# Kernel optimization log

Measured on AMD Instinct MI355X. Metric: run time of the kernel, lower is better.

## Reference

```python
import jax, jax.numpy as jnp
import numpy as np

PI = 3.141592653589793
WINDOW = 16


def multi_pose(y):
    """Intensity-moment pose extraction (MultiPoseExtraction).
    y: [..., h, w] nonnegative intensities.
    Returns mu [...,2,1] (x,y centroid in pixel coords), U [...,2,2] with
    row 0 = principal eigenvector, and eigenvalues (L1, L2), L1 >= L2,
    via the same closed-form 2x2 eigen solve used in congregate_pose."""
    h, w = y.shape[-2], y.shape[-1]
    X = jnp.arange(w, dtype=y.dtype)            # column (x) coordinate
    Y = jnp.arange(h, dtype=y.dtype)[:, None]   # row (y) coordinate
    tot = jnp.sum(y, axis=(-2, -1), keepdims=True)
    p = y / (tot + 1e-8)
    mu_x = jnp.sum(p * X, axis=(-2, -1))
    mu_y = jnp.sum(p * Y, axis=(-2, -1))
    dx = X - mu_x[..., None, None]
    dy = Y - mu_y[..., None, None]
    cxx = jnp.sum(p * dx * dx, axis=(-2, -1))
    cyy = jnp.sum(p * dy * dy, axis=(-2, -1))
    cxy = jnp.sum(p * dx * dy, axis=(-2, -1))
    tr = cxx + cyy
    det = cxx * cyy - cxy * cxy
    disc = jnp.sqrt(jax.nn.relu(tr * tr - 4.0 * det))
    L1 = (tr + disc) / 2.0
    L2 = (tr - disc) / 2.0
    v1 = jnp.stack([L1 - cyy, cxy], axis=-1)
    v1 = v1 / jnp.maximum(jnp.linalg.norm(v1, axis=-1, keepdims=True), 1e-12)
    v2 = jnp.stack([-v1[..., 1], v1[..., 0]], axis=-1)
    U = jnp.stack([v1, v2], axis=-2)            # [...,2,2], U[...,0,:] = v1
    mu = jnp.stack([mu_x, mu_y], axis=-1)[..., None]  # [...,2,1]
    return mu, U, (L1, L2)


def deep_hog_forward(x, window):
    B, C, H, W = x.shape  # C == 1
    w = window
    mean = jnp.mean(x)
    # nn.Unfold with kernel=stride=w -> non-overlapping windows, row-major order
    blocks = x.reshape(B, H // w, w, W // w, w)
    blocks = blocks.transpose(0, 1, 3, 2, 4).reshape(B, -1, w, w)  # [B, L, w, w]
    block_means = blocks.mean(axis=(-2, -1))                        # [B, L]

    mu_global, _, _ = multi_pose(x)             # [B, 1, 2, 1]
    mu_W, U, (L1, L2) = multi_pose(blocks)      # [B,L,2,1], [B,L,2,2], [B,L]

    conf = ((L1 / L2)[..., None] - 1.0) * (block_means[..., None] / mean)
    conf = 20.0 * (jax.nn.sigmoid(conf) - 0.5)  # [B, L, 1]
    orient = U[:, :, 0, :] * conf               # [B, L, 2]

    # congregate_pose: closed-form top eigenvector of sum of outer products
    M = jnp.einsum('bli,blj->bij', orient, orient)  # [B,2,2]
    T_ = M[:, 0, 0] + M[:, 1, 1]
    D = M[:, 0, 0] * M[:, 1, 1] - M[:, 0, 1] * M[:, 1, 0]
    L1g = (T_ + jnp.sqrt(jax.nn.relu(T_ * T_ - 4.0 * D))) / 2.0
    v1 = jnp.stack([L1g - M[:, 1, 1], M[:, 1, 0]], axis=1)
    V = v1 / jnp.maximum(jnp.linalg.norm(v1, axis=1, keepdims=True), 1e-12)  # [B,2]

    output = jnp.concatenate([mu_W[:, :, :, 0], orient], axis=2)  # [B, L, 4]
    U_global = V[:, None, :]                                      # [B, 1, 2]

    # anti_pose_transformation
    eps = 1e-4
    rot_lambda = jnp.fmod(
        jnp.arctan2(U_global[:, 0, 1], U_global[:, 0, 0] + eps) + 2.0 * PI, PI)
    diff = PI / 2.0 - rot_lambda                 # [B]
    c, s = jnp.cos(diff), jnp.sin(diff)
    R = jnp.stack([jnp.stack([c, -s], axis=-1),
                   jnp.stack([s, c], axis=-1)], axis=-2)  # [B,2,2]
    mu = mu_global[:, 0, :, 0]                            # [B,2]
    mu_T = mu * jnp.array([1.0 / W, 1.0 / H], x.dtype) - 0.5   # normalize, - mu_R
    mu_T = mu_T * jnp.array([2.0, -2.0], x.dtype)               # flip_y_loc
    theta = jnp.concatenate([R, mu_T[:, :, None]], axis=2)      # [B,2,3]

    return output, blocks, mu_global, U_global, theta


def setup_inputs() -> dict:
    key = jax.random.key(0)
    x = jax.random.uniform(key, (64, 1, 1024, 1024), dtype=jnp.float32)
    return {"x": x}


def reference(x):
    return deep_hog_forward(x, WINDOW)
```

## Files before the change

kernel.cpp:

```cpp
#include <hip/hip_runtime.h>
#include <math.h>

#define PI_F 3.14159265358979323846f

#define OUT_OUTPUT   0
#define OUT_BLOCKS   1048576
#define OUT_MU       68157440
#define OUT_UG       68157568
#define OUT_THETA    68157696

#define WS_A   0
#define WS_B   1048576
#define WS_IMG 2097152
#define WS_M   2097216

__global__ __launch_bounds__(256) void k1_blocks(const float* __restrict__ x,
                                                 float* __restrict__ out,
                                                 float* __restrict__ ws) {
    __shared__ float lds[16 * 264];
    const int t = threadIdx.x;
    const int colstrip = blockIdx.x;
    const int rowstrip = blockIdx.y;
    const int b = blockIdx.z;

    const float4* x4 = reinterpret_cast<const float4*>(x)
                     + (size_t)b * 262144 + (size_t)rowstrip * 4096 + colstrip * 64;
    #pragma unroll
    for (int i = 0; i < 4; ++i) {
        int pos4 = i * 256 + t;
        int row  = pos4 >> 6;
        int col4 = pos4 & 63;
        float4 v = x4[row * 256 + col4];
        int ib = col4 >> 2;
        int c4 = (col4 & 3) << 2;
        *reinterpret_cast<float4*>(&lds[ib * 264 + row * 16 + c4]) = v;
    }
    __syncthreads();

    float* outB = out + OUT_BLOCKS
                + ((size_t)b * 4096 + rowstrip * 64 + colstrip * 16) * 256;
    #pragma unroll
    for (int i = 0; i < 4; ++i) {
        int pos4 = i * 256 + t;
        int ib  = pos4 >> 6;
        int off = (pos4 & 63) << 2;
        float4 v = *reinterpret_cast<const float4*>(&lds[ib * 264 + off]);
        reinterpret_cast<float4*>(outB)[pos4] = v;
    }

    const int ib = t >> 4;
    const int c  = t & 15;
    float s0 = 0.f, s1y = 0.f, s2yy = 0.f;
    #pragma unroll
    for (int r = 0; r < 16; ++r) {
        float v  = lds[ib * 264 + r * 16 + c];
        float rf = (float)r;
        s0   += v;
        s1y  += rf * v;
        s2yy += rf * rf * v;
    }
    float cf   = (float)c;
    float s1x  = cf * s0;
    float s2xx = cf * cf * s0;
    float s2xy = cf * s1y;
    #pragma unroll
    for (int m = 1; m <= 8; m <<= 1) {
        s0   += __shfl_xor(s0,   m);
        s1x  += __shfl_xor(s1x,  m);
        s1y  += __shfl_xor(s1y,  m);
        s2xx += __shfl_xor(s2xx, m);
        s2yy += __shfl_xor(s2yy, m);
        s2xy += __shfl_xor(s2xy, m);
    }
    if (c == 0) {
        float denom = s0 + 1e-8f;
        float inv   = 1.0f / denom;
        float mu_x = s1x * inv, mu_y = s1y * inv;
        float cxx = (s2xx - 2.f * mu_x * s1x + mu_x * mu_x * s0) * inv;
        float cyy = (s2yy - 2.f * mu_y * s1y + mu_y * mu_y * s0) * inv;
        float cxy = (s2xy - mu_x * s1y - mu_y * s1x + mu_x * mu_y * s0) * inv;
        float tr  = cxx + cyy;
        float det = cxx * cyy - cxy * cxy;
        float disc = sqrtf(fmaxf(tr * tr - 4.f * det, 0.f));
        float L1 = 0.5f * (tr + disc), L2 = 0.5f * (tr - disc);
        float v1x = L1 - cyy, v1y = cxy;
        float n = fmaxf(sqrtf(v1x * v1x + v1y * v1y), 1e-12f);
        v1x /= n; v1y /= n;
        float rm1 = L1 / L2 - 1.0f;

        int l = rowstrip * 64 + colstrip * 16 + ib;
        size_t gbl = (size_t)b * 4096 + l;
        out[OUT_OUTPUT + gbl * 4 + 0] = mu_x;
        out[OUT_OUTPUT + gbl * 4 + 1] = mu_y;

        float X0 = (float)(colstrip * 256 + ib * 16);
        float Y0 = (float)(rowstrip * 16);
        float4 wa = make_float4(v1x, v1y, rm1, s0 * (1.f / 256.f));
        float4 wb = make_float4(s0, s1x + X0 * s0, s1y + Y0 * s0, 0.f);
        reinterpret_cast<float4*>(ws + WS_A)[gbl] = wa;
        reinterpret_cast<float4*>(ws + WS_B)[gbl] = wb;
    }
}

__global__ __launch_bounds__(256) void k2_global(float* __restrict__ out,
                                                 float* __restrict__ ws) {
    __shared__ float red[12];
    const int b = blockIdx.x;
    const int t = threadIdx.x;
    float s0 = 0.f, gx = 0.f, gy = 0.f;
    const float4* wb = reinterpret_cast<const float4*>(ws + WS_B) + (size_t)b * 4096;
    #pragma unroll
    for (int k = 0; k < 16; ++k) {
        float4 v = wb[t + k * 256];
        s0 += v.x; gx += v.y; gy += v.z;
    }
    #pragma unroll
    for (int m = 1; m <= 32; m <<= 1) {
        s0 += __shfl_xor(s0, m);
        gx += __shfl_xor(gx, m);
        gy += __shfl_xor(gy, m);
    }
    int w = t >> 6;
    if ((t & 63) == 0) { red[w] = s0; red[4 + w] = gx; red[8 + w] = gy; }
    __syncthreads();
    if (t == 0) {
        float S0 = red[0] + red[1] + red[2] + red[3];
        float GX = red[4] + red[5] + red[6] + red[7];
        float GY = red[8] + red[9] + red[10] + red[11];
        float inv = 1.0f / (S0 + 1e-8f);
        out[OUT_MU + b * 2 + 0] = GX * inv;
        out[OUT_MU + b * 2 + 1] = GY * inv;
        ws[WS_IMG + b] = S0;
    }
}

__global__ __launch_bounds__(256) void k3_orient(float* __restrict__ out,
                                                 float* __restrict__ ws) {
    __shared__ float red[12];
    const int b = blockIdx.x;
    const int t = threadIdx.x;
    float tot = 0.f;
    #pragma unroll
    for (int k = 0; k < 64; ++k) tot += ws[WS_IMG + k];
    float invmean = 67108864.0f / tot;
    float m00 = 0.f, m01 = 0.f, m11 = 0.f;
    const float4* wa = reinterpret_cast<const float4*>(ws + WS_A) + (size_t)b * 4096;
    #pragma unroll
    for (int k = 0; k < 16; ++k) {
        int l = t + k * 256;
        float4 v = wa[l];
        float z = v.z * (v.w * invmean);
        float conf = 20.f * (1.f / (1.f + expf(-z)) - 0.5f);
        float ox = v.x * conf, oy = v.y * conf;
        size_t gbl = (size_t)b * 4096 + l;
        *reinterpret_cast<float2*>(&out[OUT_OUTPUT + gbl * 4 + 2]) = make_float2(ox, oy);
        m00 += ox * ox; m01 += ox * oy; m11 += oy * oy;
    }
    #pragma unroll
    for (int m = 1; m <= 32; m <<= 1) {
        m00 += __shfl_xor(m00, m);
        m01 += __shfl_xor(m01, m);
        m11 += __shfl_xor(m11, m);
    }
    int w = t >> 6;
    if ((t & 63) == 0) { red[w] = m00; red[4 + w] = m01; red[8 + w] = m11; }
    __syncthreads();
    if (t == 0) {
        float M00 = red[0] + red[1] + red[2] + red[3];
        float M01 = red[4] + red[5] + red[6] + red[7];
        float M11 = red[8] + red[9] + red[10] + red[11];
        reinterpret_cast<float4*>(ws + WS_M)[b] = make_float4(M00, M01, M11, 0.f);
    }
}

__global__ void k4_theta(float* __restrict__ out, const float* __restrict__ ws) {
    int b = threadIdx.x;
    if (b >= 64) return;
    float4 M = reinterpret_cast<const float4*>(ws + WS_M)[b];
    float T = M.x + M.z;
    float D = M.x * M.z - M.y * M.y;
    float L1g = 0.5f * (T + sqrtf(fmaxf(T * T - 4.f * D, 0.f)));
    float vx = L1g - M.z, vy = M.y;
    float n = fmaxf(sqrtf(vx * vx + vy * vy), 1e-12f);
    float Vx = vx / n, Vy = vy / n;
    out[OUT_UG + b * 2 + 0] = Vx;
    out[OUT_UG + b * 2 + 1] = Vy;
    float rot = fmodf(atan2f(Vy, Vx + 1e-4f) + 2.f * PI_F, PI_F);
    float diff = 0.5f * PI_F - rot;
    float cc = cosf(diff), ssn = sinf(diff);
    float mu_x = out[OUT_MU + b * 2 + 0];
    float mu_y = out[OUT_MU + b * 2 + 1];
    float mtx = (mu_x * (1.f / 1024.f) - 0.5f) * 2.f;
    float mty = (mu_y * (1.f / 1024.f) - 0.5f) * (-2.f);
    out[OUT_THETA + b * 6 + 0] = cc;
    out[OUT_THETA + b * 6 + 1] = -ssn;
    out[OUT_THETA + b * 6 + 2] = mtx;
    out[OUT_THETA + b * 6 + 3] = ssn;
    out[OUT_THETA + b * 6 + 4] = cc;
    out[OUT_THETA + b * 6 + 5] = mty;
}

extern "C" void kernel_launch(void* const* d_in, const int* in_sizes, int n_in,
                              void* d_out, int out_size, void* d_ws, size_t ws_size,
                              hipStream_t stream) {
    const float* x = (const float*)d_in[0];
    float* out = (float*)d_out;
    float* ws  = (float*)d_ws;
    dim3 g1(4, 64, 64);
    k1_blocks<<<g1, 256, 0, stream>>>(x, out, ws);
    k2_global<<<64, 256, 0, stream>>>(out, ws);
    k3_orient<<<64, 256, 0, stream>>>(out, ws);
    k4_theta<<<1, 64, 0, stream>>>(out, ws);
}
```

Before: 447.1 us.

## Fuse global reduction, orientation and theta kernels; pre-reduce per-workgroup partials

Folds k2, k3 and k4 into a single kernel and has k1 reduce its 16 block partials in LDS into one per-workgroup entry, so the global stage reads 16K partials instead of 262K. The blocks copy now uses nontemporal stores, and output rows are written as full float4 rows rather than split writes. The aim is to remove two launches and cut workspace traffic. The cost is that every workgroup redundantly reads all partials to get the global total. The main k1 traffic, dominated by the 256 MB input read and 256 MB write, is unchanged.

```diff
diff --git a/kernel.cpp b/kernel.cpp
--- a/kernel.cpp
+++ b/kernel.cpp
@@ -2,6 +2,8 @@
 #include <math.h>
 
 #define PI_F 3.14159265358979323846f
+
+typedef float f4 __attribute__((ext_vector_type(4)));
 
 #define OUT_OUTPUT   0
 #define OUT_BLOCKS   1048576
@@ -10,30 +12,30 @@
 #define OUT_THETA    68157696
 
 #define WS_A   0
-#define WS_B   1048576
-#define WS_IMG 2097152
-#define WS_M   2097216
+#define WS_C   1048576
+#define WS_P   1310720
 
 __global__ __launch_bounds__(256) void k1_blocks(const float* __restrict__ x,
                                                  float* __restrict__ out,
                                                  float* __restrict__ ws) {
     __shared__ float lds[16 * 264];
+    __shared__ float redP[3][16];
     const int t = threadIdx.x;
     const int colstrip = blockIdx.x;
     const int rowstrip = blockIdx.y;
     const int b = blockIdx.z;
 
-    const float4* x4 = reinterpret_cast<const float4*>(x)
-                     + (size_t)b * 262144 + (size_t)rowstrip * 4096 + colstrip * 64;
+    const f4* x4 = reinterpret_cast<const f4*>(x)
+                 + (size_t)b * 262144 + (size_t)rowstrip * 4096 + colstrip * 64;
     #pragma unroll
     for (int i = 0; i < 4; ++i) {
         int pos4 = i * 256 + t;
         int row  = pos4 >> 6;
         int col4 = pos4 & 63;
-        float4 v = x4[row * 256 + col4];
+        f4 v = x4[row * 256 + col4];
         int ib = col4 >> 2;
         int c4 = (col4 & 3) << 2;
-        *reinterpret_cast<float4*>(&lds[ib * 264 + row * 16 + c4]) = v;
+        *reinterpret_cast<f4*>(&lds[ib * 264 + row * 16 + c4]) = v;
     }
     __syncthreads();
 
@@ -44,8 +46,8 @@
         int pos4 = i * 256 + t;
         int ib  = pos4 >> 6;
         int off = (pos4 & 63) << 2;
-        float4 v = *reinterpret_cast<const float4*>(&lds[ib * 264 + off]);
-        reinterpret_cast<float4*>(outB)[pos4] = v;
+        f4 v = *reinterpret_cast<const f4*>(&lds[ib * 264 + off]);
+        __builtin_nontemporal_store(v, reinterpret_cast<f4*>(outB) + pos4);
     }
 
     const int ib = t >> 4;
@@ -90,70 +92,78 @@
 
         int l = rowstrip * 64 + colstrip * 16 + ib;
         size_t gbl = (size_t)b * 4096 + l;
-        out[OUT_OUTPUT + gbl * 4 + 0] = mu_x;
-        out[OUT_OUTPUT + gbl * 4 + 1] = mu_y;
+        f4 wa = {v1x, v1y, mu_x, mu_y};
+        reinterpret_cast<f4*>(ws + WS_A)[gbl] = wa;
+        ws[WS_C + gbl] = rm1 * (s0 * (1.f / 256.f));
 
         float X0 = (float)(colstrip * 256 + ib * 16);
         float Y0 = (float)(rowstrip * 16);
-        float4 wa = make_float4(v1x, v1y, rm1, s0 * (1.f / 256.f));
-        float4 wb = make_float4(s0, s1x + X0 * s0, s1y + Y0 * s0, 0.f);
-        reinterpret_cast<float4*>(ws + WS_A)[gbl] = wa;
-        reinterpret_cast<float4*>(ws + WS_B)[gbl] = wb;
+        redP[0][ib] = s0;
+        redP[1][ib] = s1x + X0 * s0;
+        redP[2][ib] = s1y + Y0 * s0;
+    }
+    __syncthreads();
+    if (t == 0) {
+        float S0 = 0.f, GX = 0.f, GY = 0.f;
+        #pragma unroll
+        for (int i = 0; i < 16; ++i) { S0 += redP[0][i]; GX += redP[1][i]; GY += redP[2][i]; }
+        int wg = (b << 8) | (rowstrip << 2) | colstrip;
+        reinterpret_cast<f4*>(ws + WS_P)[wg] = (f4){S0, GX, GY, 0.f};
     }
 }
 
-__global__ __launch_bounds__(256) void k2_global(float* __restrict__ out,
-                                                 float* __restrict__ ws) {
-    __shared__ float red[12];
+__global__ __launch_bounds__(256) void k23_orient(float* __restrict__ out,
+                                                  const float* __restrict__ ws) {
+    __shared__ float red[16];
+    __shared__ float bc[1];
     const int b = blockIdx.x;
     const int t = threadIdx.x;
-    float s0 = 0.f, gx = 0.f, gy = 0.f;
-    const float4* wb = reinterpret_cast<const float4*>(ws + WS_B) + (size_t)b * 4096;
-    #pragma unroll
-    for (int k = 0; k < 16; ++k) {
-        float4 v = wb[t + k * 256];
-        s0 += v.x; gx += v.y; gy += v.z;
+
+    const f4* wp = reinterpret_cast<const f4*>(ws + WS_P);
+    float tS0 = 0.f, iS0 = 0.f, igx = 0.f, igy = 0.f;
+    #pragma unroll
+    for (int k = 0; k < 64; ++k) {
+        f4 v = wp[k * 256 + t];
+        tS0 += v.x;
+        if (k == b) { iS0 += v.x; igx += v.y; igy += v.z; }
     }
     #pragma unroll
     for (int m = 1; m <= 32; m <<= 1) {
-        s0 += __shfl_xor(s0, m);
-        gx += __shfl_xor(gx, m);
-        gy += __shfl_xor(gy, m);
-    }
-    int w = t >> 6;
-    if ((t & 63) == 0) { red[w] = s0; red[4 + w] = gx; red[8 + w] = gy; }
-    __syncthreads();
+        tS0 += __shfl_xor(tS0, m);
+        iS0 += __shfl_xor(iS0, m);
+        igx += __shfl_xor(igx, m);
+        igy += __shfl_xor(igy, m);
+    }
+    const int w = t >> 6;
+    if ((t & 63) == 0) { red[w] = tS0; red[4 + w] = iS0; red[8 + w] = igx; red[12 + w] = igy; }
+    __syncthreads();
+    float mu_x = 0.f, mu_y = 0.f;
     if (t == 0) {
-        float S0 = red[0] + red[1] + red[2] + red[3];
-        float GX = red[4] + red[5] + red[6] + red[7];
-        float GY = red[8] + red[9] + red[10] + red[11];
-        float inv = 1.0f / (S0 + 1e-8f);
-        out[OUT_MU + b * 2 + 0] = GX * inv;
-        out[OUT_MU + b * 2 + 1] = GY * inv;
-        ws[WS_IMG + b] = S0;
-    }
-}
-
-__global__ __launch_bounds__(256) void k3_orient(float* __restrict__ out,
-                                                 float* __restrict__ ws) {
-    __shared__ float red[12];
-    const int b = blockIdx.x;
-    const int t = threadIdx.x;
-    float tot = 0.f;
-    #pragma unroll
-    for (int k = 0; k < 64; ++k) tot += ws[WS_IMG + k];
-    float invmean = 67108864.0f / tot;
+        float T  = red[0] + red[1] + red[2] + red[3];
+        float S  = red[4] + red[5] + red[6] + red[7];
+        float GX = red[8] + red[9] + red[10] + red[11];
+        float GY = red[12] + red[13] + red[14] + red[15];
+        float inv = 1.0f / (S + 1e-8f);
+        mu_x = GX * inv; mu_y = GY * inv;
+        out[OUT_MU + b * 2 + 0] = mu_x;
+        out[OUT_MU + b * 2 + 1] = mu_y;
+        bc[0] = T;
+    }
+    __syncthreads();
+    const float invmean = 67108864.0f / bc[0];
+
     float m00 = 0.f, m01 = 0.f, m11 = 0.f;
-    const float4* wa = reinterpret_cast<const float4*>(ws + WS_A) + (size_t)b * 4096;
+    const f4*    wa   = reinterpret_cast<const f4*>(ws + WS_A) + (size_t)b * 4096;
+    const float* wc   = ws + WS_C + (size_t)b * 4096;
+    f4*          out4 = reinterpret_cast<f4*>(out + OUT_OUTPUT) + (size_t)b * 4096;
     #pragma unroll
     for (int k = 0; k < 16; ++k) {
         int l = t + k * 256;
-        float4 v = wa[l];
-        float z = v.z * (v.w * invmean);
+        f4 a = wa[l];
+        float z = wc[l] * invmean;
         float conf = 20.f * (1.f / (1.f + expf(-z)) - 0.5f);
-        float ox = v.x * conf, oy = v.y * conf;
-        size_t gbl = (size_t)b * 4096 + l;
-        *reinterpret_cast<float2*>(&out[OUT_OUTPUT + gbl * 4 + 2]) = make_float2(ox, oy);
+        float ox = a.x * conf, oy = a.y * conf;
+        out4[l] = (f4){a.z, a.w, ox, oy};
         m00 += ox * ox; m01 += ox * oy; m11 += oy * oy;
     }
     #pragma unroll
@@ -162,42 +172,33 @@
         m01 += __shfl_xor(m01, m);
         m11 += __shfl_xor(m11, m);
     }
-    int w = t >> 6;
     if ((t & 63) == 0) { red[w] = m00; red[4 + w] = m01; red[8 + w] = m11; }
     __syncthreads();
+
     if (t == 0) {
         float M00 = red[0] + red[1] + red[2] + red[3];
         float M01 = red[4] + red[5] + red[6] + red[7];
         float M11 = red[8] + red[9] + red[10] + red[11];
-        reinterpret_cast<float4*>(ws + WS_M)[b] = make_float4(M00, M01, M11, 0.f);
-    }
-}
-
-__global__ void k4_theta(float* __restrict__ out, const float* __restrict__ ws) {
-    int b = threadIdx.x;
-    if (b >= 64) return;
-    float4 M = reinterpret_cast<const float4*>(ws + WS_M)[b];
-    float T = M.x + M.z;
-    float D = M.x * M.z - M.y * M.y;
-    float L1g = 0.5f * (T + sqrtf(fmaxf(T * T - 4.f * D, 0.f)));
-    float vx = L1g - M.z, vy = M.y;
-    float n = fmaxf(sqrtf(vx * vx + vy * vy), 1e-12f);
-    float Vx = vx / n, Vy = vy / n;
-    out[OUT_UG + b * 2 + 0] = Vx;
-    out[OUT_UG + b * 2 + 1] = Vy;
-    float rot = fmodf(atan2f(Vy, Vx + 1e-4f) + 2.f * PI_F, PI_F);
-    float diff = 0.5f * PI_F - rot;
-    float cc = cosf(diff), ssn = sinf(diff);
-    float mu_x = out[OUT_MU + b * 2 + 0];
-    float mu_y = out[OUT_MU + b * 2 + 1];
-    float mtx = (mu_x * (1.f / 1024.f) - 0.5f) * 2.f;
-    float mty = (mu_y * (1.f / 1024.f) - 0.5f) * (-2.f);
-    out[OUT_THETA + b * 6 + 0] = cc;
-    out[OUT_THETA + b * 6 + 1] = -ssn;
-    out[OUT_THETA + b * 6 + 2] = mtx;
-    out[OUT_THETA + b * 6 + 3] = ssn;
-    out[OUT_THETA + b * 6 + 4] = cc;
-    out[OUT_THETA + b * 6 + 5] = mty;
+        float T = M00 + M11;
+        float D = M00 * M11 - M01 * M01;
+        float L1g = 0.5f * (T + sqrtf(fmaxf(T * T - 4.f * D, 0.f)));
+        float vx = L1g - M11, vy = M01;
+        float n = fmaxf(sqrtf(vx * vx + vy * vy), 1e-12f);
+        float Vx = vx / n, Vy = vy / n;
+        out[OUT_UG + b * 2 + 0] = Vx;
+        out[OUT_UG + b * 2 + 1] = Vy;
+        float rot = fmodf(atan2f(Vy, Vx + 1e-4f) + 2.f * PI_F, PI_F);
+        float diff = 0.5f * PI_F - rot;
+        float cc = cosf(diff), ssn = sinf(diff);
+        float mtx = (mu_x * (1.f / 1024.f) - 0.5f) * 2.f;
+        float mty = (mu_y * (1.f / 1024.f) - 0.5f) * (-2.f);
+        out[OUT_THETA + b * 6 + 0] = cc;
+        out[OUT_THETA + b * 6 + 1] = -ssn;
+        out[OUT_THETA + b * 6 + 2] = mtx;
+        out[OUT_THETA + b * 6 + 3] = ssn;
+        out[OUT_THETA + b * 6 + 4] = cc;
+        out[OUT_THETA + b * 6 + 5] = mty;
+    }
 }
 
 extern "C" void kernel_launch(void* const* d_in, const int* in_sizes, int n_in,
@@ -208,7 +209,5 @@
     float* ws  = (float*)d_ws;
     dim3 g1(4, 64, 64);
     k1_blocks<<<g1, 256, 0, stream>>>(x, out, ws);
-    k2_global<<<64, 256, 0, stream>>>(out, ws);
-    k3_orient<<<64, 256, 0, stream>>>(out, ws);
-    k4_theta<<<1, 64, 0, stream>>>(out, ws);
+    k23_orient<<<64, 256, 0, stream>>>(out, ws);
 }
```

Measured after the change: 457.0 us. 2.2% more time.
